# Performance work log

Measured on AMD Instinct MI355X. Metric: run time of the kernel, lower is better.

The kernel has to match this reference:

```python
import math
import jax, jax.numpy as jnp
import numpy as np

B, N, D = 2, 2048, 1024
FEAT, DK = 256, 64
N_WAVE, N_PROJ, N_STD = 4, 4, 8
H = N_WAVE + N_PROJ + N_STD


def setup_inputs() -> dict:
    key = jax.random.key(0)
    ks = jax.random.split(key, 16)
    sF = 1.0 / math.sqrt(FEAT)
    sD = 1.0 / math.sqrt(D)
    return {
        "x": jax.random.normal(ks[0], (B, N, D), jnp.float32),
        "features": jax.random.normal(ks[1], (B, N, FEAT), jnp.float32),
        "mask": jnp.ones((B, N, N), dtype=bool),
        # wave heads: fixed random projections [n_wave, feature_dim, d_k], init randn/sqrt(feature_dim)
        "wave_proj": jax.random.normal(ks[2], (N_WAVE, FEAT, DK), jnp.float32) * sF,
        # learned projection heads (no bias)
        "pq_w": jax.random.normal(ks[3], (N_PROJ, FEAT, DK), jnp.float32) * sF,
        "pk_w": jax.random.normal(ks[4], (N_PROJ, FEAT, DK), jnp.float32) * sF,
        # standard heads Q/K projections (with bias)
        "std_q_w": jax.random.normal(ks[5], (D, N_STD * DK), jnp.float32) * sD,
        "std_q_b": jnp.zeros((N_STD * DK,), jnp.float32),
        "std_k_w": jax.random.normal(ks[6], (D, N_STD * DK), jnp.float32) * sD,
        "std_k_b": jnp.zeros((N_STD * DK,), jnp.float32),
        # value and output projections
        "v_w": jax.random.normal(ks[7], (D, H * DK), jnp.float32) * sD,
        "v_b": jnp.zeros((H * DK,), jnp.float32),
        "out_w": jax.random.normal(ks[8], (H * DK, D), jnp.float32) * (1.0 / math.sqrt(H * DK)),
        "out_b": jnp.zeros((D,), jnp.float32),
    }


def reference(x, features, mask, wave_proj, pq_w, pk_w, std_q_w, std_q_b,
              std_k_w, std_k_b, v_w, v_b, out_w, out_b):
    scale = 1.0 / math.sqrt(DK)

    # V: [B, H, N, DK]
    V = (x @ v_w + v_b).reshape(B, N, H, DK).transpose(0, 2, 1, 3)

    # wave heads: fixed projection of features, self dot-product
    wp = jnp.einsum('bnf,hfk->bhnk', features, wave_proj)          # [B, n_wave, N, DK]
    wave_scores = jnp.einsum('bhnk,bhmk->bhnm', wp, wp) * scale

    # learned projection heads: separate Q/K projections of features
    pq = jnp.einsum('bnf,hfk->bhnk', features, pq_w)
    pk = jnp.einsum('bnf,hfk->bhnk', features, pk_w)
    proj_scores = jnp.einsum('bhnk,bhmk->bhnm', pq, pk) * scale

    # standard heads: Q/K from x
    Q = (x @ std_q_w + std_q_b).reshape(B, N, N_STD, DK).transpose(0, 2, 1, 3)
    K = (x @ std_k_w + std_k_b).reshape(B, N, N_STD, DK).transpose(0, 2, 1, 3)
    std_scores = jnp.einsum('bhnk,bhmk->bhnm', Q, K) * scale

    # head order matches torch: wave, proj, std
    scores = jnp.concatenate([wave_scores, proj_scores, std_scores], axis=1)  # [B, H, N, N]
    scores = jnp.where(mask[:, None, :, :], scores, -jnp.inf)
    attn = jax.nn.softmax(scores, axis=-1)

    out = jnp.einsum('bhnm,bhmk->bhnk', attn, V)       # [B, H, N, DK]
    out = out.transpose(0, 2, 1, 3).reshape(B, N, H * DK)
    return out @ out_w + out_b
```

## Files before the change

kernel.cpp:

```cpp
#include <hip/hip_runtime.h>
#include <hip/hip_bf16.h>

typedef __hip_bfloat16 bf16;

#define BB     2
#define NSEQ   2048
#define DMODEL 1024
#define FEATD  256
#define DKH    64
#define NHEAD  16
#define KT     64
#define QSC    (0.125f * 1.44269504f)

typedef __bf16 bf16x8 __attribute__((ext_vector_type(8)));
typedef float  f32x4  __attribute__((ext_vector_type(4)));
typedef float  f32x16 __attribute__((ext_vector_type(16)));

__device__ __forceinline__ unsigned short f2bf(float f) {
    union { __hip_bfloat16 h; unsigned short u; } cv;
    cv.h = __float2bfloat16(f);
    return cv.u;
}

__device__ __forceinline__ unsigned int cvtpk(float lo, float hi) {
    unsigned int r;
    asm("v_cvt_pk_bf16_f32 %0, %1, %2" : "=v"(r) : "v"(lo), "v"(hi));
    return r;
}
__device__ __forceinline__ void plswap(unsigned int& a, unsigned int& b) {
    asm volatile("v_permlane32_swap_b32 %0, %1" : "+v"(a), "+v"(b));
}

__device__ __forceinline__
void transpose_body(const float* __restrict__ src, bf16* __restrict__ dst,
                    int N, int dst_ld, int row0, int kt, int nt)
{
    __shared__ float T[64][65];
    const int tid = threadIdx.x;
    const int r = tid >> 2, c0 = (tid & 3) * 16;
#pragma unroll
    for (int j = 0; j < 16; j += 4) {
        float4 v = *reinterpret_cast<const float4*>(src + (size_t)(kt * 64 + r) * N + nt * 64 + c0 + j);
        T[r][c0 + j] = v.x; T[r][c0 + j + 1] = v.y; T[r][c0 + j + 2] = v.z; T[r][c0 + j + 3] = v.w;
    }
    __syncthreads();
    const int orow = row0 + nt * 64 + r;
    unsigned int u[8];
#pragma unroll
    for (int j = 0; j < 8; ++j)
        u[j] = (unsigned int)f2bf(T[c0 + 2 * j][r]) | ((unsigned int)f2bf(T[c0 + 2 * j + 1][r]) << 16);
    uint4* dp = reinterpret_cast<uint4*>(dst + (size_t)orow * dst_ld + kt * 64 + c0);
    dp[0] = make_uint4(u[0], u[1], u[2], u[3]);
    dp[1] = make_uint4(u[4], u[5], u[6], u[7]);
}

__global__ __launch_bounds__(256)
void prep_all(const float* __restrict__ v_w, const float* __restrict__ q_w,
              const float* __restrict__ k_w, const float* __restrict__ wave_w,
              const float* __restrict__ pqw, const float* __restrict__ pkw,
              const float* __restrict__ out_w,
              const float* __restrict__ xsrc, const float* __restrict__ fsrc,
              bf16* __restrict__ Wcat, bf16* __restrict__ Fcat, bf16* __restrict__ OwT,
              bf16* __restrict__ xdst, bf16* __restrict__ fdst)
{
    const int x = blockIdx.x, y = blockIdx.y;
    if (blockIdx.z == 0) {
        const float* src; int N, row0, nt;
        if (y < 16)      { src = v_w; N = 1024; row0 = 0;    nt = y; }
        else if (y < 24) { src = q_w; N = 512;  row0 = 1024; nt = y - 16; }
        else             { src = k_w; N = 512;  row0 = 1536; nt = y - 24; }
        transpose_body(src, Wcat, N, 1024, row0, x, nt);
    } else if (blockIdx.z == 1) {
        if (y < 12) {
            if (x >= 4) return;
            const float* src; int row0;
            if (y < 4)      { src = wave_w + (size_t)y * FEATD * DKH;    row0 = 64 * y; }
            else if (y < 8) { src = pqw + (size_t)(y - 4) * FEATD * DKH; row0 = 256 + 64 * (y - 4); }
            else            { src = pkw + (size_t)(y - 8) * FEATD * DKH; row0 = 512 + 64 * (y - 8); }
            transpose_body(src, Fcat, 64, 256, row0, x, 0);
        } else if (y < 28) {
            transpose_body(out_w, OwT, 1024, 1024, 0, x, y - 12);
        }
    } else {
        const int n8x = BB * NSEQ * DMODEL / 8, n8f = BB * NSEQ * FEATD / 8;
        const int total = n8x + n8f;
        const int bid = y * 16 + x;
        for (int i = bid * 256 + threadIdx.x; i < total; i += 512 * 256) {
            const float* s; bf16* d; int j;
            if (i < n8x) { s = xsrc; d = xdst; j = i; }
            else         { s = fsrc; d = fdst; j = i - n8x; }
            float4 a = reinterpret_cast<const float4*>(s)[2 * j];
            float4 b = reinterpret_cast<const float4*>(s)[2 * j + 1];
            uint4 o;
            o.x = (unsigned int)f2bf(a.x) | ((unsigned int)f2bf(a.y) << 16);
            o.y = (unsigned int)f2bf(a.z) | ((unsigned int)f2bf(a.w) << 16);
            o.z = (unsigned int)f2bf(b.x) | ((unsigned int)f2bf(b.y) << 16);
            o.w = (unsigned int)f2bf(b.z) | ((unsigned int)f2bf(b.w) << 16);
            reinterpret_cast<uint4*>(d)[j] = o;
        }
    }
}

__global__ __launch_bounds__(256)
void mfma_gemm(const bf16* __restrict__ A0, const bf16* __restrict__ BT0, int K0, int mode0,
               const bf16* __restrict__ A1, const bf16* __restrict__ BT1, int K1, int mode1, int ylim1,
               const float* __restrict__ bias0, const float* __restrict__ bias1,
               const float* __restrict__ bias2,
               bf16* __restrict__ Qd, bf16* __restrict__ Kd, bf16* __restrict__ Vd,
               float* __restrict__ Fout)
{
    const bf16* A; const bf16* BT; int K; int mode;
    if (blockIdx.z == 0) { A = A0; BT = BT0; K = K0; mode = mode0; }
    else {
        if ((int)blockIdx.y >= ylim1) return;
        A = A1; BT = BT1; K = K1; mode = mode1;
    }

    __shared__ __align__(16) unsigned char As[2][128 * 128];
    __shared__ __align__(16) unsigned char Bs[2][128 * 128];

    const int tid = threadIdx.x;
    const int wv = tid >> 6, lane = tid & 63;
    const int lg = lane >> 4, lc = lane & 15;
    const int wr = wv >> 1, wc = wv & 1;
    const int bm0 = blockIdx.x * 128, bn0 = blockIdx.y * 128;
    const size_t Kb = (size_t)K * 2;

    const int srow_in = lane >> 3;
    const int slot_lin = lane & 7;

    f32x4 acc[4][4];
#pragma unroll
    for (int mi = 0; mi < 4; ++mi)
#pragma unroll
        for (int ni = 0; ni < 4; ++ni)
            acc[mi][ni] = (f32x4){0.f, 0.f, 0.f, 0.f};

    const int nk = K >> 6;

#define GEMM_STAGE(ksv, bi) do {                                               \
    const size_t kb_ = (size_t)(ksv) * 128;                                    \
    _Pragma("unroll")                                                          \
    for (int t = 0; t < 4; ++t) {                                              \
        const int chunk = t * 4 + wv;                                          \
        const int r = chunk * 8 + srow_in;                                     \
        const int s = slot_lin ^ (r & 7);                                      \
        __builtin_amdgcn_global_load_lds(                                      \
            (const __attribute__((address_space(1))) void*)((const char*)A + (size_t)(bm0 + r) * Kb + kb_ + s * 16), \
            (__attribute__((address_space(3))) void*)(As[bi] + chunk * 1024), 16, 0, 0); \
        __builtin_amdgcn_global_load_lds(                                      \
            (const __attribute__((address_space(1))) void*)((const char*)BT + (size_t)(bn0 + r) * Kb + kb_ + s * 16), \
            (__attribute__((address_space(3))) void*)(Bs[bi] + chunk * 1024), 16, 0, 0); \
    }                                                                          \
} while (0)

    GEMM_STAGE(0, 0);
    if (nk > 1) GEMM_STAGE(1, 1);

    for (int ks = 0; ks < nk; ++ks) {
        if (ks < nk - 1) asm volatile("s_waitcnt vmcnt(8)" ::: "memory");
        else             asm volatile("s_waitcnt vmcnt(0)" ::: "memory");
        __builtin_amdgcn_s_barrier();
        const unsigned char* Ac = As[ks & 1];
        const unsigned char* Bc = Bs[ks & 1];
#pragma unroll
        for (int kk = 0; kk < 2; ++kk) {
            const int boff = (kk * 64 + lg * 16) ^ ((lc & 7) << 4);
            bf16x8 af[4], bfr[4];
#pragma unroll
            for (int mi = 0; mi < 4; ++mi)
                af[mi] = *reinterpret_cast<const bf16x8*>(Ac + (wr * 64 + mi * 16 + lc) * 128 + boff);
#pragma unroll
            for (int ni = 0; ni < 4; ++ni)
                bfr[ni] = *reinterpret_cast<const bf16x8*>(Bc + (wc * 64 + ni * 16 + lc) * 128 + boff);
#pragma unroll
            for (int mi = 0; mi < 4; ++mi)
#pragma unroll
                for (int ni = 0; ni < 4; ++ni)
                    acc[mi][ni] = __builtin_amdgcn_mfma_f32_16x16x32_bf16(af[mi], bfr[ni], acc[mi][ni], 0, 0, 0);
        }
        __builtin_amdgcn_s_barrier();
        if (ks + 2 < nk) GEMM_STAGE(ks + 2, ks & 1);
    }
#undef GEMM_STAGE

#pragma unroll
    for (int mi = 0; mi < 4; ++mi) {
        const int m = bm0 + wr * 64 + mi * 16 + lg * 4;
#pragma unroll
        for (int ni = 0; ni < 4; ++ni) {
            const int n = bn0 + wc * 64 + ni * 16 + lc;
            if (mode == 2) {
                const float bv = bias0[n];
#pragma unroll
                for (int r = 0; r < 4; ++r)
                    Fout[(size_t)(m + r) * DMODEL + n] = acc[mi][ni][r] + bv;
            } else if (mode == 0) {
                const int dk = n & 63;
                if (n < 1024) {
                    const int h = n >> 6;
                    const float bv = bias0[n];
                    const int b = m >> 11, nn0 = m & (NSEQ - 1);
                    uint2 pk;
                    pk.x = (unsigned int)f2bf(acc[mi][ni][0] + bv) | ((unsigned int)f2bf(acc[mi][ni][1] + bv) << 16);
                    pk.y = (unsigned int)f2bf(acc[mi][ni][2] + bv) | ((unsigned int)f2bf(acc[mi][ni][3] + bv) << 16);
                    *reinterpret_cast<uint2*>(Vd + (((size_t)b * NHEAD + h) * DKH + dk) * NSEQ + nn0) = pk;
                } else {
                    bf16* dstp; int h; float bv; float sc;
                    if (n < 1536) { dstp = Qd; h = 8 + ((n - 1024) >> 6); bv = bias1[n - 1024]; sc = QSC; }
                    else          { dstp = Kd; h = 8 + ((n - 1536) >> 6); bv = bias2[n - 1536]; sc = 1.0f; }
#pragma unroll
                    for (int r = 0; r < 4; ++r) {
                        const int mm = m + r, b = mm >> 11, nn = mm & (NSEQ - 1);
                        dstp[(((size_t)b * NHEAD + h) * NSEQ + nn) * DKH + dk] = __float2bfloat16((acc[mi][ni][r] + bv) * sc);
                    }
                }
            } else {
                bf16* d0; bf16* d1 = nullptr; int h;
                bool q0;
                if (n < 256)      { h = n >> 6;             d0 = Qd; d1 = Kd; q0 = true; }
                else if (n < 512) { h = 4 + ((n - 256) >> 6); d0 = Qd; q0 = true; }
                else              { h = 4 + ((n - 512) >> 6); d0 = Kd; q0 = false; }
                const int dk = n & 63;
#pragma unroll
                for (int r = 0; r < 4; ++r) {
                    const int mm = m + r, b = mm >> 11, nn = mm & (NSEQ - 1);
                    const size_t idx = (((size_t)b * NHEAD + h) * NSEQ + nn) * DKH + dk;
                    d0[idx] = __float2bfloat16(q0 ? acc[mi][ni][r] * QSC : acc[mi][ni][r]);
                    if (d1) d1[idx] = __float2bfloat16(acc[mi][ni][r]);
                }
            }
        }
    }
}

__global__ __launch_bounds__(256, 2)
void flash_mfma(const bf16* __restrict__ Q, const bf16* __restrict__ K,
                const bf16* __restrict__ VT, bf16* __restrict__ O)
{
    __shared__ __align__(16) unsigned char lds[3][16384];

    const int tid  = threadIdx.x;
    const int wv   = tid >> 6;
    const int lane = tid & 63;
    const int ql   = lane & 31;
    const int hi   = lane >> 5;

    const int bh = blockIdx.x;
    const int b  = bh >> 4, h = bh & 15;
    const int qbase = blockIdx.y * 128 + wv * 32;

    const bf16* Qb  = Q + (size_t)bh * NSEQ * DKH;
    const char* Kb  = (const char*)(K + (size_t)bh * NSEQ * DKH);
    const char* VTb = (const char*)(VT + (size_t)bh * DKH * NSEQ);

    bf16x8 qf[4];
#pragma unroll
    for (int dt = 0; dt < 4; ++dt)
        qf[dt] = *reinterpret_cast<const bf16x8*>(
            (const char*)Qb + (size_t)(qbase + ql) * 128 + dt * 32 + hi * 16);

    f32x16 oacc[2];
    f32x16 zro;
#pragma unroll
    for (int i = 0; i < 16; ++i) { oacc[0][i] = 0.f; oacc[1][i] = 0.f; zro[i] = 0.f; }
    float l = 0.f;

    const int srow  = lane >> 3;
    const int sslot = lane & 7;
    const int sxor  = (sslot ^ srow) << 4;
    const int kr0 = wv * 8 + srow, kr1 = 32 + wv * 8 + srow;
    const char* ks0 = Kb + (size_t)kr0 * 128 + sxor;
    const char* ks1 = Kb + (size_t)kr1 * 128 + sxor;
    const char* vs0 = VTb + (size_t)kr0 * (NSEQ * 2) + sxor;
    const char* vs1 = VTb + (size_t)kr1 * (NSEQ * 2) + sxor;
    const int ldk0 = wv * 1024, ldk1 = 4096 + wv * 1024;
    const int ldv0 = 8192 + wv * 1024, ldv1 = 12288 + wv * 1024;

#define FLASH_ISSUE(t, bufi) do {                                              \
    unsigned char* Lb = lds[bufi];                                             \
    __builtin_amdgcn_global_load_lds(                                          \
        (const __attribute__((address_space(1))) void*)(ks0 + (size_t)(t) * 8192), \
        (__attribute__((address_space(3))) void*)(Lb + ldk0), 16, 0, 0);       \
    __builtin_amdgcn_global_load_lds(                                          \
        (const __attribute__((address_space(1))) void*)(ks1 + (size_t)(t) * 8192), \
        (__attribute__((address_space(3))) void*)(Lb + ldk1), 16, 0, 0);       \
    __builtin_amdgcn_global_load_lds(                                          \
        (const __attribute__((address_space(1))) void*)(vs0 + (size_t)(t) * 128),  \
        (__attribute__((address_space(3))) void*)(Lb + ldv0), 16, 0, 0);       \
    __builtin_amdgcn_global_load_lds(                                          \
        (const __attribute__((address_space(1))) void*)(vs1 + (size_t)(t) * 128),  \
        (__attribute__((address_space(3))) void*)(Lb + ldv1), 16, 0, 0);       \
} while (0)

    const int swq = ql & 7;

    FLASH_ISSUE(0, 0);
    FLASH_ISSUE(1, 1);

    for (int kb = 0; kb < NSEQ / KT; ++kb) {
        if (kb < NSEQ / KT - 1) {
            asm volatile("s_waitcnt vmcnt(4)" ::: "memory");
        } else {
            asm volatile("s_waitcnt vmcnt(0)" ::: "memory");
        }
        __builtin_amdgcn_s_barrier();
        if (kb + 2 < NSEQ / KT) FLASH_ISSUE(kb + 2, (kb + 2) % 3);
        unsigned char* cbase = lds[kb % 3];

        f32x16 s[2];
        __builtin_amdgcn_s_setprio(1);
#pragma unroll
        for (int kt = 0; kt < 2; ++kt) {
            f32x16 acc;
#pragma unroll
            for (int dt = 0; dt < 4; ++dt) {
                bf16x8 kf = *(const bf16x8*)(cbase + (kt * 32 + ql) * 128 + (((dt * 2 + hi) ^ swq) << 4));
                acc = __builtin_amdgcn_mfma_f32_32x32x16_bf16(kf, qf[dt], dt == 0 ? zro : acc, 0, 0, 0);
            }
            s[kt] = acc;
        }
        __builtin_amdgcn_s_setprio(0);

#pragma unroll
        for (int kt = 0; kt < 2; ++kt)
#pragma unroll
            for (int i = 0; i < 16; ++i)
                s[kt][i] = __builtin_amdgcn_exp2f(s[kt][i]);
        float u[8];
#pragma unroll
        for (int i = 0; i < 8; ++i)
            u[i] = (s[0][i] + s[0][i + 8]) + (s[1][i] + s[1][i + 8]);
        l += ((u[0] + u[1]) + (u[2] + u[3])) + ((u[4] + u[5]) + (u[6] + u[7]));

        unsigned int w[2][4][2];
#pragma unroll
        for (int kt = 0; kt < 2; ++kt)
#pragma unroll
            for (int g = 0; g < 4; ++g) {
                w[kt][g][0] = cvtpk(s[kt][4 * g + 0], s[kt][4 * g + 1]);
                w[kt][g][1] = cvtpk(s[kt][4 * g + 2], s[kt][4 * g + 3]);
            }
        bf16x8 pfr[4];
#pragma unroll
        for (int ks = 0; ks < 4; ++ks) {
            const int kt = ks >> 1, g0 = (ks & 1) * 2;
            unsigned int a0 = w[kt][g0][0], b0 = w[kt][g0 + 1][0];
            unsigned int a1 = w[kt][g0][1], b1 = w[kt][g0 + 1][1];
            plswap(a0, b0);
            plswap(a1, b1);
            union { unsigned int u[4]; bf16x8 v; } pk;
            pk.u[0] = a0; pk.u[1] = a1; pk.u[2] = b0; pk.u[3] = b1;
            pfr[ks] = pk.v;
        }

        __builtin_amdgcn_s_setprio(1);
#pragma unroll
        for (int dti = 0; dti < 2; ++dti)
#pragma unroll
            for (int ks = 0; ks < 4; ++ks) {
                bf16x8 vf = *(const bf16x8*)(cbase + 8192 + (dti * 32 + ql) * 128 + (((ks * 2 + hi) ^ swq) << 4));
                oacc[dti] = __builtin_amdgcn_mfma_f32_32x32x16_bf16(vf, pfr[ks], oacc[dti], 0, 0, 0);
            }
        __builtin_amdgcn_s_setprio(0);
    }
#undef FLASH_ISSUE

    l += __shfl_xor(l, 32);
    const float linv = 1.0f / l;
    bf16* Ob = O + (((size_t)b * NSEQ + qbase + ql) * NHEAD + h) * DKH;
#pragma unroll
    for (int dti = 0; dti < 2; ++dti)
#pragma unroll
        for (int g = 0; g < 4; ++g) {
            uint2 pk;
            pk.x = cvtpk(oacc[dti][4 * g + 0] * linv, oacc[dti][4 * g + 1] * linv);
            pk.y = cvtpk(oacc[dti][4 * g + 2] * linv, oacc[dti][4 * g + 3] * linv);
            *reinterpret_cast<uint2*>(Ob + dti * 32 + 8 * g + 4 * hi) = pk;
        }
}

extern "C" void kernel_launch(void* const* d_in, const int* in_sizes, int n_in,
                              void* d_out, int out_size, void* d_ws, size_t ws_size,
                              hipStream_t stream) {
    const float* x         = (const float*)d_in[0];
    const float* features  = (const float*)d_in[1];
    const float* wave_proj = (const float*)d_in[3];
    const float* pq_w      = (const float*)d_in[4];
    const float* pk_w      = (const float*)d_in[5];
    const float* std_q_w   = (const float*)d_in[6];
    const float* std_q_b   = (const float*)d_in[7];
    const float* std_k_w   = (const float*)d_in[8];
    const float* std_k_b   = (const float*)d_in[9];
    const float* v_w       = (const float*)d_in[10];
    const float* v_b       = (const float*)d_in[11];
    const float* out_w     = (const float*)d_in[12];
    const float* out_b     = (const float*)d_in[13];
    float* out = (float*)d_out;

    char* ws = (char*)d_ws;
    const size_t MB = 1024 * 1024;
    bf16* Qws   = (bf16*)(ws);
    bf16* Kws   = (bf16*)(ws + 8 * MB);
    bf16* VTws  = (bf16*)(ws + 16 * MB);
    bf16* xb    = (bf16*)(ws + 24 * MB);
    bf16* Ows   = (bf16*)(ws + 24 * MB);
    bf16* fb    = (bf16*)(ws + 32 * MB);
    bf16* WcatT = (bf16*)(ws + 34 * MB);
    bf16* FcatT = (bf16*)(ws + 38 * MB);
    bf16* OwT   = (bf16*)(ws + 39 * MB);

    dim3 blk(256);
    prep_all<<<dim3(16, 32, 3), blk, 0, stream>>>(v_w, std_q_w, std_k_w,
                                                  wave_proj, pq_w, pk_w, out_w,
                                                  x, features,
                                                  WcatT, FcatT, OwT, xb, fb);
    mfma_gemm<<<dim3(32, 16, 2), blk, 0, stream>>>(xb, WcatT, DMODEL, 0,
                                                   fb, FcatT, FEATD, 1, 6,
                                                   v_b, std_q_b, std_k_b,
                                                   Qws, Kws, VTws, nullptr);
    flash_mfma<<<dim3(BB * NHEAD, NSEQ / 128), blk, 0, stream>>>(Qws, Kws, VTws, Ows);
    mfma_gemm<<<dim3(32, 8, 1), blk, 0, stream>>>(Ows, OwT, DMODEL, 2,
                                                  nullptr, nullptr, 0, 0, 0,
                                                  out_b, nullptr, nullptr,
                                                  nullptr, nullptr, nullptr, out);
}
```

Baseline: 111.9 us.

## Process two query tiles per wave in flash attention to reuse K/V fragments

Each wave now handles two 32-row query tiles, so each block covers 256 queries and the grid's y dimension is halved. Every K and V fragment read from LDS feeds two MFMAs instead of one, which halves the K/V global and LDS traffic per query and doubles the MFMA work between barriers. The cost is roughly double the accumulator and score registers, so launch bounds drop to one block per CU hint. The grid shrinks to 256 blocks, which may leave the GPU's compute units underused.

```diff
diff --git a/kernel.cpp b/kernel.cpp
--- a/kernel.cpp
+++ b/kernel.cpp
@@ -234,7 +234,7 @@
     }
 }
 
-__global__ __launch_bounds__(256, 2)
+__global__ __launch_bounds__(256, 1)
 void flash_mfma(const bf16* __restrict__ Q, const bf16* __restrict__ K,
                 const bf16* __restrict__ VT, bf16* __restrict__ O)
 {
@@ -248,23 +248,31 @@
 
     const int bh = blockIdx.x;
     const int b  = bh >> 4, h = bh & 15;
-    const int qbase = blockIdx.y * 128 + wv * 32;
+    const int qbase0 = blockIdx.y * 256 + wv * 32;
+    const int qbase1 = qbase0 + 128;
 
     const bf16* Qb  = Q + (size_t)bh * NSEQ * DKH;
     const char* Kb  = (const char*)(K + (size_t)bh * NSEQ * DKH);
     const char* VTb = (const char*)(VT + (size_t)bh * DKH * NSEQ);
 
-    bf16x8 qf[4];
-#pragma unroll
-    for (int dt = 0; dt < 4; ++dt)
-        qf[dt] = *reinterpret_cast<const bf16x8*>(
-            (const char*)Qb + (size_t)(qbase + ql) * 128 + dt * 32 + hi * 16);
-
-    f32x16 oacc[2];
+    bf16x8 qf0[4], qf1[4];
+#pragma unroll
+    for (int dt = 0; dt < 4; ++dt) {
+        qf0[dt] = *reinterpret_cast<const bf16x8*>(
+            (const char*)Qb + (size_t)(qbase0 + ql) * 128 + dt * 32 + hi * 16);
+        qf1[dt] = *reinterpret_cast<const bf16x8*>(
+            (const char*)Qb + (size_t)(qbase1 + ql) * 128 + dt * 32 + hi * 16);
+    }
+
+    f32x16 oacc0[2], oacc1[2];
     f32x16 zro;
 #pragma unroll
-    for (int i = 0; i < 16; ++i) { oacc[0][i] = 0.f; oacc[1][i] = 0.f; zro[i] = 0.f; }
-    float l = 0.f;
+    for (int i = 0; i < 16; ++i) {
+        oacc0[0][i] = 0.f; oacc0[1][i] = 0.f;
+        oacc1[0][i] = 0.f; oacc1[1][i] = 0.f;
+        zro[i] = 0.f;
+    }
+    float l0 = 0.f, l1 = 0.f;
 
     const int srow  = lane >> 3;
     const int sslot = lane & 7;
@@ -308,50 +316,81 @@
         if (kb + 2 < NSEQ / KT) FLASH_ISSUE(kb + 2, (kb + 2) % 3);
         unsigned char* cbase = lds[kb % 3];
 
-        f32x16 s[2];
+        f32x16 s0[2], s1[2];
         __builtin_amdgcn_s_setprio(1);
 #pragma unroll
         for (int kt = 0; kt < 2; ++kt) {
-            f32x16 acc;
+            f32x16 a0, a1;
 #pragma unroll
             for (int dt = 0; dt < 4; ++dt) {
                 bf16x8 kf = *(const bf16x8*)(cbase + (kt * 32 + ql) * 128 + (((dt * 2 + hi) ^ swq) << 4));
-                acc = __builtin_amdgcn_mfma_f32_32x32x16_bf16(kf, qf[dt], dt == 0 ? zro : acc, 0, 0, 0);
-            }
-            s[kt] = acc;
+                a0 = __builtin_amdgcn_mfma_f32_32x32x16_bf16(kf, qf0[dt], dt == 0 ? zro : a0, 0, 0, 0);
+                a1 = __builtin_amdgcn_mfma_f32_32x32x16_bf16(kf, qf1[dt], dt == 0 ? zro : a1, 0, 0, 0);
+            }
+            s0[kt] = a0; s1[kt] = a1;
         }
         __builtin_amdgcn_s_setprio(0);
 
 #pragma unroll
         for (int kt = 0; kt < 2; ++kt)
 #pragma unroll
-            for (int i = 0; i < 16; ++i)
-                s[kt][i] = __builtin_amdgcn_exp2f(s[kt][i]);
-        float u[8];
-#pragma unroll
-        for (int i = 0; i < 8; ++i)
-            u[i] = (s[0][i] + s[0][i + 8]) + (s[1][i] + s[1][i + 8]);
-        l += ((u[0] + u[1]) + (u[2] + u[3])) + ((u[4] + u[5]) + (u[6] + u[7]));
-
-        unsigned int w[2][4][2];
-#pragma unroll
-        for (int kt = 0; kt < 2; ++kt)
-#pragma unroll
-            for (int g = 0; g < 4; ++g) {
-                w[kt][g][0] = cvtpk(s[kt][4 * g + 0], s[kt][4 * g + 1]);
-                w[kt][g][1] = cvtpk(s[kt][4 * g + 2], s[kt][4 * g + 3]);
-            }
-        bf16x8 pfr[4];
-#pragma unroll
-        for (int ks = 0; ks < 4; ++ks) {
-            const int kt = ks >> 1, g0 = (ks & 1) * 2;
-            unsigned int a0 = w[kt][g0][0], b0 = w[kt][g0 + 1][0];
-            unsigned int a1 = w[kt][g0][1], b1 = w[kt][g0 + 1][1];
-            plswap(a0, b0);
-            plswap(a1, b1);
-            union { unsigned int u[4]; bf16x8 v; } pk;
-            pk.u[0] = a0; pk.u[1] = a1; pk.u[2] = b0; pk.u[3] = b1;
-            pfr[ks] = pk.v;
+            for (int i = 0; i < 16; ++i) {
+                s0[kt][i] = __builtin_amdgcn_exp2f(s0[kt][i]);
+                s1[kt][i] = __builtin_amdgcn_exp2f(s1[kt][i]);
+            }
+        {
+            float u0[8], u1[8];
+#pragma unroll
+            for (int i = 0; i < 8; ++i) {
+                u0[i] = (s0[0][i] + s0[0][i + 8]) + (s0[1][i] + s0[1][i + 8]);
+                u1[i] = (s1[0][i] + s1[0][i + 8]) + (s1[1][i] + s1[1][i + 8]);
+            }
+            l0 += ((u0[0] + u0[1]) + (u0[2] + u0[3])) + ((u0[4] + u0[5]) + (u0[6] + u0[7]));
+            l1 += ((u1[0] + u1[1]) + (u1[2] + u1[3])) + ((u1[4] + u1[5]) + (u1[6] + u1[7]));
+        }
+
+        bf16x8 pfr0[4], pfr1[4];
+        {
+            unsigned int w[2][4][2];
+#pragma unroll
+            for (int kt = 0; kt < 2; ++kt)
+#pragma unroll
+                for (int g = 0; g < 4; ++g) {
+                    w[kt][g][0] = cvtpk(s0[kt][4 * g + 0], s0[kt][4 * g + 1]);
+                    w[kt][g][1] = cvtpk(s0[kt][4 * g + 2], s0[kt][4 * g + 3]);
+                }
+#pragma unroll
+            for (int ks = 0; ks < 4; ++ks) {
+                const int kt = ks >> 1, g0 = (ks & 1) * 2;
+                unsigned int a0 = w[kt][g0][0], b0 = w[kt][g0 + 1][0];
+                unsigned int a1 = w[kt][g0][1], b1 = w[kt][g0 + 1][1];
+                plswap(a0, b0);
+                plswap(a1, b1);
+                union { unsigned int u[4]; bf16x8 v; } pk;
+                pk.u[0] = a0; pk.u[1] = a1; pk.u[2] = b0; pk.u[3] = b1;
+                pfr0[ks] = pk.v;
+            }
+        }
+        {
+            unsigned int w[2][4][2];
+#pragma unroll
+            for (int kt = 0; kt < 2; ++kt)
+#pragma unroll
+                for (int g = 0; g < 4; ++g) {
+                    w[kt][g][0] = cvtpk(s1[kt][4 * g + 0], s1[kt][4 * g + 1]);
+                    w[kt][g][1] = cvtpk(s1[kt][4 * g + 2], s1[kt][4 * g + 3]);
+                }
+#pragma unroll
+            for (int ks = 0; ks < 4; ++ks) {
+                const int kt = ks >> 1, g0 = (ks & 1) * 2;
+                unsigned int a0 = w[kt][g0][0], b0 = w[kt][g0 + 1][0];
+                unsigned int a1 = w[kt][g0][1], b1 = w[kt][g0 + 1][1];
+                plswap(a0, b0);
+                plswap(a1, b1);
+                union { unsigned int u[4]; bf16x8 v; } pk;
+                pk.u[0] = a0; pk.u[1] = a1; pk.u[2] = b0; pk.u[3] = b1;
+                pfr1[ks] = pk.v;
+            }
         }
 
         __builtin_amdgcn_s_setprio(1);
@@ -360,23 +399,30 @@
 #pragma unroll
             for (int ks = 0; ks < 4; ++ks) {
                 bf16x8 vf = *(const bf16x8*)(cbase + 8192 + (dti * 32 + ql) * 128 + (((ks * 2 + hi) ^ swq) << 4));
-                oacc[dti] = __builtin_amdgcn_mfma_f32_32x32x16_bf16(vf, pfr[ks], oacc[dti], 0, 0, 0);
+                oacc0[dti] = __builtin_amdgcn_mfma_f32_32x32x16_bf16(vf, pfr0[ks], oacc0[dti], 0, 0, 0);
+                oacc1[dti] = __builtin_amdgcn_mfma_f32_32x32x16_bf16(vf, pfr1[ks], oacc1[dti], 0, 0, 0);
             }
         __builtin_amdgcn_s_setprio(0);
     }
 #undef FLASH_ISSUE
 
-    l += __shfl_xor(l, 32);
-    const float linv = 1.0f / l;
-    bf16* Ob = O + (((size_t)b * NSEQ + qbase + ql) * NHEAD + h) * DKH;
+    l0 += __shfl_xor(l0, 32);
+    l1 += __shfl_xor(l1, 32);
+    const float li0 = 1.0f / l0;
+    const float li1 = 1.0f / l1;
+    bf16* Ob0 = O + (((size_t)b * NSEQ + qbase0 + ql) * NHEAD + h) * DKH;
+    bf16* Ob1 = O + (((size_t)b * NSEQ + qbase1 + ql) * NHEAD + h) * DKH;
 #pragma unroll
     for (int dti = 0; dti < 2; ++dti)
 #pragma unroll
         for (int g = 0; g < 4; ++g) {
             uint2 pk;
-            pk.x = cvtpk(oacc[dti][4 * g + 0] * linv, oacc[dti][4 * g + 1] * linv);
-            pk.y = cvtpk(oacc[dti][4 * g + 2] * linv, oacc[dti][4 * g + 3] * linv);
-            *reinterpret_cast<uint2*>(Ob + dti * 32 + 8 * g + 4 * hi) = pk;
+            pk.x = cvtpk(oacc0[dti][4 * g + 0] * li0, oacc0[dti][4 * g + 1] * li0);
+            pk.y = cvtpk(oacc0[dti][4 * g + 2] * li0, oacc0[dti][4 * g + 3] * li0);
+            *reinterpret_cast<uint2*>(Ob0 + dti * 32 + 8 * g + 4 * hi) = pk;
+            pk.x = cvtpk(oacc1[dti][4 * g + 0] * li1, oacc1[dti][4 * g + 1] * li1);
+            pk.y = cvtpk(oacc1[dti][4 * g + 2] * li1, oacc1[dti][4 * g + 3] * li1);
+            *reinterpret_cast<uint2*>(Ob1 + dti * 32 + 8 * g + 4 * hi) = pk;
         }
 }
 
@@ -419,7 +465,7 @@
                                                    fb, FcatT, FEATD, 1, 6,
                                                    v_b, std_q_b, std_k_b,
                                                    Qws, Kws, VTws, nullptr);
-    flash_mfma<<<dim3(BB * NHEAD, NSEQ / 128), blk, 0, stream>>>(Qws, Kws, VTws, Ows);
+    flash_mfma<<<dim3(BB * NHEAD, NSEQ / 256), blk, 0, stream>>>(Qws, Kws, VTws, Ows);
     mfma_gemm<<<dim3(32, 8, 1), blk, 0, stream>>>(Ows, OwT, DMODEL, 2,
                                                   nullptr, nullptr, 0, 0, 0,
                                                   out_b, nullptr, nullptr,
```

New measurement: 117.6 us. 5.1% more time.

## Widen flash attention blocks to 512 threads covering 256 query rows

Applied to the files above, without the earlier changes.

The flash attention kernel now runs 8 waves per block, each owning 32 query rows, so one block covers 256 queries and shares each K/V tile staged in LDS among twice as many waves. Each thread issues half as many async global-to-LDS loads per tile, and the wait count is adjusted to match. This halves the number of blocks and the total K/V traffic from global memory. In exchange there are fewer blocks, 256 instead of 512, with larger barriers, so occupancy and latency hiding may suffer.

```diff
diff --git a/kernel.cpp b/kernel.cpp
--- a/kernel.cpp
+++ b/kernel.cpp
@@ -234,7 +234,7 @@
     }
 }
 
-__global__ __launch_bounds__(256, 2)
+__global__ __launch_bounds__(512, 1)
 void flash_mfma(const bf16* __restrict__ Q, const bf16* __restrict__ K,
                 const bf16* __restrict__ VT, bf16* __restrict__ O)
 {
@@ -248,7 +248,7 @@
 
     const int bh = blockIdx.x;
     const int b  = bh >> 4, h = bh & 15;
-    const int qbase = blockIdx.y * 128 + wv * 32;
+    const int qbase = blockIdx.y * 256 + wv * 32;
 
     const bf16* Qb  = Q + (size_t)bh * NSEQ * DKH;
     const char* Kb  = (const char*)(K + (size_t)bh * NSEQ * DKH);
@@ -266,31 +266,22 @@
     for (int i = 0; i < 16; ++i) { oacc[0][i] = 0.f; oacc[1][i] = 0.f; zro[i] = 0.f; }
     float l = 0.f;
 
-    const int srow  = lane >> 3;
-    const int sslot = lane & 7;
-    const int sxor  = (sslot ^ srow) << 4;
-    const int kr0 = wv * 8 + srow, kr1 = 32 + wv * 8 + srow;
-    const char* ks0 = Kb + (size_t)kr0 * 128 + sxor;
-    const char* ks1 = Kb + (size_t)kr1 * 128 + sxor;
-    const char* vs0 = VTb + (size_t)kr0 * (NSEQ * 2) + sxor;
-    const char* vs1 = VTb + (size_t)kr1 * (NSEQ * 2) + sxor;
-    const int ldk0 = wv * 1024, ldk1 = 4096 + wv * 1024;
-    const int ldv0 = 8192 + wv * 1024, ldv1 = 12288 + wv * 1024;
+    const int srow  = tid >> 3;
+    const int sslot = tid & 7;
+    const int sxor  = (sslot ^ (srow & 7)) << 4;
+    const char* ksrc = Kb + (size_t)srow * 128 + sxor;
+    const char* vsrc = VTb + (size_t)srow * (NSEQ * 2) + sxor;
+    const int ldk = wv * 1024;
+    const int ldv = 8192 + wv * 1024;
 
 #define FLASH_ISSUE(t, bufi) do {                                              \
     unsigned char* Lb = lds[bufi];                                             \
     __builtin_amdgcn_global_load_lds(                                          \
-        (const __attribute__((address_space(1))) void*)(ks0 + (size_t)(t) * 8192), \
-        (__attribute__((address_space(3))) void*)(Lb + ldk0), 16, 0, 0);       \
+        (const __attribute__((address_space(1))) void*)(ksrc + (size_t)(t) * 8192), \
+        (__attribute__((address_space(3))) void*)(Lb + ldk), 16, 0, 0);        \
     __builtin_amdgcn_global_load_lds(                                          \
-        (const __attribute__((address_space(1))) void*)(ks1 + (size_t)(t) * 8192), \
-        (__attribute__((address_space(3))) void*)(Lb + ldk1), 16, 0, 0);       \
-    __builtin_amdgcn_global_load_lds(                                          \
-        (const __attribute__((address_space(1))) void*)(vs0 + (size_t)(t) * 128),  \
-        (__attribute__((address_space(3))) void*)(Lb + ldv0), 16, 0, 0);       \
-    __builtin_amdgcn_global_load_lds(                                          \
-        (const __attribute__((address_space(1))) void*)(vs1 + (size_t)(t) * 128),  \
-        (__attribute__((address_space(3))) void*)(Lb + ldv1), 16, 0, 0);       \
+        (const __attribute__((address_space(1))) void*)(vsrc + (size_t)(t) * 128),  \
+        (__attribute__((address_space(3))) void*)(Lb + ldv), 16, 0, 0);        \
 } while (0)
 
     const int swq = ql & 7;
@@ -300,7 +291,7 @@
 
     for (int kb = 0; kb < NSEQ / KT; ++kb) {
         if (kb < NSEQ / KT - 1) {
-            asm volatile("s_waitcnt vmcnt(4)" ::: "memory");
+            asm volatile("s_waitcnt vmcnt(2)" ::: "memory");
         } else {
             asm volatile("s_waitcnt vmcnt(0)" ::: "memory");
         }
@@ -419,7 +410,7 @@
                                                    fb, FcatT, FEATD, 1, 6,
                                                    v_b, std_q_b, std_k_b,
                                                    Qws, Kws, VTws, nullptr);
-    flash_mfma<<<dim3(BB * NHEAD, NSEQ / 128), blk, 0, stream>>>(Qws, Kws, VTws, Ows);
+    flash_mfma<<<dim3(BB * NHEAD, NSEQ / 256), dim3(512), 0, stream>>>(Qws, Kws, VTws, Ows);
     mfma_gemm<<<dim3(32, 8, 1), blk, 0, stream>>>(Ows, OwT, DMODEL, 2,
                                                   nullptr, nullptr, 0, 0, 0,
                                                   out_b, nullptr, nullptr,
```

Measured after the change: 108.8 us. -2.8%, faster.
